# Optimization experiments

Hardware: AMD Instinct MI355X
Metric: run time of the kernel (lower is better)

The kernel has to match this reference:

```python
import jax, jax.numpy as jnp
import numpy as np

N = 50000
E = 1_600_000
D_IN = 128
D_H = 64
D_E = 32
NEG_SLOPE = 0.2


def setup_inputs() -> dict:
    key = jax.random.key(0)
    ks = jax.random.split(key, 20)
    p = lambda k, sh: jax.random.normal(k, sh, jnp.float32) * 0.1
    return {
        "x": jax.random.normal(ks[0], (N, D_IN), jnp.float32),
        "edge_index": jax.random.randint(ks[1], (2, E), 0, N, jnp.int32),
        "edge_attr": jax.random.normal(ks[2], (E, D_E), jnp.float32),
        # layer 1 params (GATv2Conv, heads=1)
        "Wl1": p(ks[3], (D_IN, D_H)), "bl1": p(ks[4], (D_H,)),
        "Wr1": p(ks[5], (D_IN, D_H)), "br1": p(ks[6], (D_H,)),
        "We1": p(ks[7], (D_E, D_H)),
        "att1": p(ks[8], (D_H,)), "bias1": p(ks[9], (D_H,)),
        # layer 2 params
        "Wl2": p(ks[10], (D_H, D_H)), "bl2": p(ks[11], (D_H,)),
        "Wr2": p(ks[12], (D_H, D_H)), "br2": p(ks[13], (D_H,)),
        "We2": p(ks[14], (D_E, D_H)),
        "att2": p(ks[15], (D_H,)), "bias2": p(ks[16], (D_H,)),
        # classifier
        "Wc": p(ks[17], (D_H, 2)), "bc": p(ks[18], (2,)),
    }


def _gatv2(x, src, dst, eattr, Wl, bl, Wr, br, We, att, bias, n):
    # x: [n, d_in]; src/dst: [Ea]; eattr: [Ea, d_e]
    xl = x @ Wl + bl                      # [n, d_h] (source transform; also message value)
    xr = x @ Wr + br                      # [n, d_h] (target transform)
    z = xl[src] + xr[dst] + eattr @ We    # [Ea, d_h]
    score = jax.nn.leaky_relu(z, NEG_SLOPE) @ att  # [Ea]
    # numerically stable softmax over incoming edges per destination node
    m = jax.ops.segment_max(score, dst, num_segments=n)
    ex = jnp.exp(score - m[dst])
    denom = jax.ops.segment_sum(ex, dst, num_segments=n)
    alpha = ex / denom[dst]               # [Ea]
    out = jax.ops.segment_sum(alpha[:, None] * xl[src], dst, num_segments=n)
    return out + bias


def reference(x, edge_index, edge_attr,
              Wl1, bl1, Wr1, br1, We1, att1, bias1,
              Wl2, bl2, Wr2, br2, We2, att2, bias2,
              Wc, bc):
    n = x.shape[0]
    src, dst = edge_index[0], edge_index[1]
    # add self-loops with fill_value='mean' (PyG default with edge_attr):
    # self-loop edge feature of node i = mean of edge_attr over edges into i
    e = edge_attr.shape[0]
    deg = jax.ops.segment_sum(jnp.ones((e,), edge_attr.dtype), dst, num_segments=n)
    loop_attr = jax.ops.segment_sum(edge_attr, dst, num_segments=n) / jnp.maximum(deg, 1.0)[:, None]
    loop = jnp.arange(n, dtype=edge_index.dtype)
    src_a = jnp.concatenate([src, loop])
    dst_a = jnp.concatenate([dst, loop])
    ea = jnp.concatenate([edge_attr, loop_attr], axis=0)

    h = jax.nn.relu(_gatv2(x, src_a, dst_a, ea, Wl1, bl1, Wr1, br1, We1, att1, bias1, n))
    # dropout(p=0.2) is identity in eval mode
    h = jax.nn.relu(_gatv2(h, src_a, dst_a, ea, Wl2, bl2, Wr2, br2, We2, att2, bias2, n))
    return h @ Wc + bc  # [n, 2]
```

## Files before the change

### kernel.cpp

```cpp
#include <hip/hip_runtime.h>
#include <hip/hip_bf16.h>

#define NEG_SLOPE 0.2f

typedef __attribute__((ext_vector_type(8))) short bf16x8;
typedef __attribute__((ext_vector_type(4))) float f32x4;

__device__ __forceinline__ float bf2f(unsigned short u) {
    return __uint_as_float((unsigned)u << 16);
}
__device__ __forceinline__ float bflo(unsigned u) { return __uint_as_float(u << 16); }
__device__ __forceinline__ float bfhi(unsigned u) { return __uint_as_float(u & 0xFFFF0000u); }
__device__ __forceinline__ unsigned short f2bf(float f) {
    unsigned b = __float_as_uint(f);
    return (unsigned short)((b + 0x7FFFu + ((b >> 16) & 1u)) >> 16);
}
__device__ __forceinline__ unsigned pack2(float lo, float hi) {
    return (unsigned)f2bf(lo) | ((unsigned)f2bf(hi) << 16);
}

__global__ void k_hist(const int* __restrict__ dst, int E, int* __restrict__ deg) {
    int e = blockIdx.x * 256 + threadIdx.x;
    if (e < E) atomicAdd(&deg[dst[e]], 1);
}

__global__ __launch_bounds__(1024) void k_scan_chunk(const int* __restrict__ deg,
                                                     int* __restrict__ start,
                                                     int* __restrict__ csum, int n) {
    __shared__ int wsum[16];
    const int lane = threadIdx.x & 63;
    const int w = threadIdx.x >> 6;
    int i = blockIdx.x * 1024 + (int)threadIdx.x;
    int v = (i < n) ? deg[i] : 0;
    int s = v;
#pragma unroll
    for (int o = 1; o < 64; o <<= 1) {
        int u = __shfl_up(s, o);
        if (lane >= o) s += u;
    }
    if (lane == 63) wsum[w] = s;
    __syncthreads();
    if (w == 0) {
        int ws = (lane < 16) ? wsum[lane] : 0;
#pragma unroll
        for (int o = 1; o < 16; o <<= 1) {
            int u = __shfl_up(ws, o);
            if (lane >= o) ws += u;
        }
        if (lane < 16) wsum[lane] = ws;
    }
    __syncthreads();
    int woff = (w == 0) ? 0 : wsum[w - 1];
    int incl = s + woff;
    if (i < n) start[i] = incl - v;
    if (threadIdx.x == 1023) csum[blockIdx.x] = incl;
}

__global__ void k_scan_top(int* __restrict__ csum, int nch, int* __restrict__ start, int n) {
    int t = threadIdx.x;
    int v = (t < nch) ? csum[t] : 0;
    int s = v;
#pragma unroll
    for (int o = 1; o < 64; o <<= 1) {
        int u = __shfl_up(s, o);
        if (t >= o) s += u;
    }
    if (t < nch) csum[t] = s - v;
    if (t == 63) start[n] = s;
}

__global__ void k_scan_apply(int* __restrict__ start, const int* __restrict__ csum, int n) {
    int i = blockIdx.x * 256 + threadIdx.x;
    if (i < n) start[i] += csum[i >> 10];
}

__global__ void k_fill(const float* __restrict__ eattr,
                       const int* __restrict__ src, const int* __restrict__ dst, int E,
                       const int* __restrict__ start, int* __restrict__ cursor,
                       int2* __restrict__ sd_sorted, unsigned short* __restrict__ eattr_s) {
    int e = blockIdx.x * 256 + threadIdx.x;
    if (e >= E) return;
    int d = dst[e];
    int idx = start[d] + atomicAdd(&cursor[d], 1);
    sd_sorted[idx] = make_int2(src[e], d);
    const float4* p = (const float4*)(eattr + (size_t)e * 32);
    uint4* q = (uint4*)(eattr_s + (size_t)idx * 32);
#pragma unroll
    for (int c = 0; c < 4; ++c) {
        const float4 a = p[2 * c], b = p[2 * c + 1];
        uint4 o;
        o.x = pack2(a.x, a.y); o.y = pack2(a.z, a.w);
        o.z = pack2(b.x, b.y); o.w = pack2(b.z, b.w);
        q[c] = o;
    }
}

__global__ __launch_bounds__(256) void k_loop_csr(
    const unsigned short* __restrict__ eattr_s, const int* __restrict__ start,
    float* __restrict__ loop_attr, int n) {
    int node = blockIdx.x * 4 + (threadIdx.x >> 6);
    int t = threadIdx.x & 63;
    if (node >= n) return;
    int a = start[node], b = start[node + 1];
    const int rpi = t >> 4;
    const int cp = t & 15;
    float ax = 0.f, ay = 0.f;
    for (int j = a + rpi; j < b; j += 4) {
        unsigned u = *(const unsigned*)&eattr_s[(size_t)j * 32 + cp * 2];
        ax += bflo(u); ay += bfhi(u);
    }
#pragma unroll
    for (int mask = 16; mask <= 32; mask <<= 1) {
        ax += __shfl_xor(ax, mask);
        ay += __shfl_xor(ay, mask);
    }
    if (t < 16) {
        float deg = fmaxf((float)(b - a), 1.f);
        float2 o = make_float2(ax / deg, ay / deg);
        *(float2*)&loop_attr[(size_t)node * 32 + cp * 2] = o;
    }
}

template <int DIN>
__global__ void k_node_transform(const float* __restrict__ h,
                                 const float* __restrict__ Wl, const float* __restrict__ bl,
                                 const float* __restrict__ Wr, const float* __restrict__ br,
                                 unsigned short* __restrict__ xlb,
                                 unsigned short* __restrict__ xrb, int n) {
    __shared__ float hs[4][DIN];
    int node0 = blockIdx.x * 4;
    int tid = threadIdx.x;
    for (int idx = tid; idx < 4 * DIN; idx += 256) {
        int ln = idx / DIN, k = idx % DIN;
        int node = node0 + ln;
        hs[ln][k] = (node < n) ? h[(long long)node * DIN + k] : 0.f;
    }
    __syncthreads();
    int ln = tid >> 6;
    int j = tid & 63;
    int node = node0 + ln;
    if (node >= n) return;
    float al = bl[j], ar = br[j];
#pragma unroll 8
    for (int k = 0; k < DIN; ++k) {
        float hv = hs[ln][k];
        al += hv * Wl[k * 64 + j];
        ar += hv * Wr[k * 64 + j];
    }
    xlb[(long long)node * 64 + j] = f2bf(al);
    xrb[(long long)node * 64 + j] = f2bf(ar);
}

__global__ __launch_bounds__(256, 2) void k_edge_score(
    const unsigned short* __restrict__ xlb, const unsigned short* __restrict__ xrb,
    const unsigned short* __restrict__ eattr_s,
    const float* __restrict__ We, const float* __restrict__ att,
    const int2* __restrict__ sd_sorted, int E,
    float* __restrict__ ex_sorted) {
    __shared__ __align__(16) short ea_frag[4][128][8];

    const int tid = threadIdx.x;
    const int ge0 = blockIdx.x * 128;
    const int w = tid >> 6, l = tid & 63;
    const int lo16 = l & 15, hi4 = l >> 4;

    int2 sd[2];
#pragma unroll
    for (int et = 0; et < 2; ++et) {
        int ge = ge0 + w * 32 + et * 16 + lo16;
        sd[et] = (ge < E) ? sd_sorted[ge] : make_int2(0, 0);
    }
    uint4 xlg[2][2], xrg[2][2];
#pragma unroll
    for (int et = 0; et < 2; ++et) {
        const size_t lbase = (size_t)sd[et].x * 64 + hi4 * 16;
        const size_t rbase = (size_t)sd[et].y * 64 + hi4 * 16;
        xlg[et][0] = *(const uint4*)&xlb[lbase];
        xlg[et][1] = *(const uint4*)&xlb[lbase + 8];
        xrg[et][0] = *(const uint4*)&xrb[rbase];
        xrg[et][1] = *(const uint4*)&xrb[rbase + 8];
    }

    {
        const int e = tid & 127;
        const int c0 = (tid >> 7) * 2;
        const int ge = ge0 + e;
        uint4 q0 = make_uint4(0, 0, 0, 0), q1 = q0;
        if (ge < E) {
            const uint4* p = (const uint4*)(eattr_s + (size_t)ge * 32 + c0 * 8);
            q0 = p[0]; q1 = p[1];
        }
        *(uint4*)&ea_frag[c0 + 0][e][0] = q0;
        *(uint4*)&ea_frag[c0 + 1][e][0] = q1;
    }

    bf16x8 afrag[4];
#pragma unroll
    for (int ct = 0; ct < 4; ++ct) {
        const int ch = (lo16 >> 2) * 16 + ct * 4 + (lo16 & 3);
#pragma unroll
        for (int j = 0; j < 8; ++j) {
            afrag[ct][j] = (short)f2bf(We[(hi4 * 8 + j) * 64 + ch]);
        }
    }
    float attf[16];
    {
        const float4 a0 = *(const float4*)&att[hi4 * 16 + 0];
        const float4 a1 = *(const float4*)&att[hi4 * 16 + 4];
        const float4 a2 = *(const float4*)&att[hi4 * 16 + 8];
        const float4 a3 = *(const float4*)&att[hi4 * 16 + 12];
        attf[0] = a0.x;  attf[1] = a0.y;  attf[2] = a0.z;  attf[3] = a0.w;
        attf[4] = a1.x;  attf[5] = a1.y;  attf[6] = a1.z;  attf[7] = a1.w;
        attf[8] = a2.x;  attf[9] = a2.y;  attf[10] = a2.z; attf[11] = a2.w;
        attf[12] = a3.x; attf[13] = a3.y; attf[14] = a3.z; attf[15] = a3.w;
    }
    __syncthreads();

    f32x4 acc[2][4];
#pragma unroll
    for (int et = 0; et < 2; ++et) {
        bf16x8 bfrag = *(const bf16x8*)&ea_frag[hi4][w * 32 + et * 16 + lo16][0];
#pragma unroll
        for (int ct = 0; ct < 4; ++ct) {
            f32x4 zero = {0.f, 0.f, 0.f, 0.f};
            acc[et][ct] = __builtin_amdgcn_mfma_f32_16x16x32_bf16(afrag[ct], bfrag, zero, 0, 0, 0);
        }
    }

#pragma unroll
    for (int et = 0; et < 2; ++et) {
        float xlf[16], xrf[16];
#pragma unroll
        for (int h = 0; h < 2; ++h) {
            const uint4 ql = xlg[et][h];
            const uint4 qr = xrg[et][h];
            xlf[h * 8 + 0] = bflo(ql.x); xlf[h * 8 + 1] = bfhi(ql.x);
            xlf[h * 8 + 2] = bflo(ql.y); xlf[h * 8 + 3] = bfhi(ql.y);
            xlf[h * 8 + 4] = bflo(ql.z); xlf[h * 8 + 5] = bfhi(ql.z);
            xlf[h * 8 + 6] = bflo(ql.w); xlf[h * 8 + 7] = bfhi(ql.w);
            xrf[h * 8 + 0] = bflo(qr.x); xrf[h * 8 + 1] = bfhi(qr.x);
            xrf[h * 8 + 2] = bflo(qr.y); xrf[h * 8 + 3] = bfhi(qr.y);
            xrf[h * 8 + 4] = bflo(qr.z); xrf[h * 8 + 5] = bfhi(qr.z);
            xrf[h * 8 + 6] = bflo(qr.w); xrf[h * 8 + 7] = bfhi(qr.w);
        }
        float part = 0.f;
#pragma unroll
        for (int ct = 0; ct < 4; ++ct) {
#pragma unroll
            for (int r = 0; r < 4; ++r) {
                const int i = ct * 4 + r;
                float zz = acc[et][ct][r] + xlf[i] + xrf[i];
                zz = (zz > 0.f) ? zz : NEG_SLOPE * zz;
                part += attf[i] * zz;
            }
        }
        part += __shfl_xor(part, 16);
        part += __shfl_xor(part, 32);
        if (l < 16) {
            int ge = ge0 + w * 32 + et * 16 + l;
            if (ge < E) ex_sorted[ge] = __expf(part);
        }
    }
}

template <bool FINAL>
__global__ __launch_bounds__(256, 2) void k_node_aggr(
    const unsigned short* __restrict__ xlb, const unsigned short* __restrict__ xrb,
    const float* __restrict__ loop_attr,
    const float* __restrict__ We, const float* __restrict__ att,
    const int* __restrict__ start,
    const int2* __restrict__ sd_sorted, const float* __restrict__ ex_sorted,
    const float* __restrict__ bias,
    const float* __restrict__ Wc, const float* __restrict__ bc,
    float* __restrict__ hout, int n) {
    __shared__ float la_s[4][32];
    const int ln = threadIdx.x >> 6;
    const int node = blockIdx.x * 4 + ln;
    const int t = threadIdx.x & 63;

    if (threadIdx.x < 128) {
        int nn = blockIdx.x * 4 + (threadIdx.x >> 5);
        int k = threadIdx.x & 31;
        la_s[threadIdx.x >> 5][k] = (nn < n) ? loop_attr[(size_t)nn * 32 + k] : 0.f;
    }
    __syncthreads();
    if (node >= n) return;

    float exl;
    {
        float zl = bf2f(xlb[(size_t)node * 64 + t]) + bf2f(xrb[(size_t)node * 64 + t]);
#pragma unroll 8
        for (int k = 0; k < 32; ++k) zl += We[k * 64 + t] * la_s[ln][k];
        zl = (zl > 0.f) ? zl : NEG_SLOPE * zl;
        float v = att[t] * zl;
#pragma unroll
        for (int mask = 1; mask <= 32; mask <<= 1) v += __shfl_xor(v, mask);
        exl = __expf(v);
    }

    const int g = t >> 3;
    const int c8 = t & 7;
    int a = start[node], b = start[node + 1];

    float acc[8] = {0.f, 0.f, 0.f, 0.f, 0.f, 0.f, 0.f, 0.f};
    float den = 0.f;
    if (g == 0) {
        const uint4 q = *(const uint4*)&xlb[(size_t)node * 64 + c8 * 8];
        acc[0] = exl * bflo(q.x); acc[1] = exl * bfhi(q.x);
        acc[2] = exl * bflo(q.y); acc[3] = exl * bfhi(q.y);
        acc[4] = exl * bflo(q.z); acc[5] = exl * bfhi(q.z);
        acc[6] = exl * bflo(q.w); acc[7] = exl * bfhi(q.w);
        den = exl;
    }
    for (int j = a; j < b; j += 64) {
        int m = b - j; if (m > 64) m = 64;
        int sj = 0; float exj = 0.f;
        if (t < m) { sj = sd_sorted[j + t].x; exj = ex_sorted[j + t]; }
        for (int i = 0; i < m; i += 16) {
            const int i0 = i + g, i1 = i + 8 + g;
            const int s0 = __shfl(sj, i0); const float e0 = __shfl(exj, i0);
            const int s1 = __shfl(sj, i1); const float e1 = __shfl(exj, i1);
            uint4 q0 = *(const uint4*)&xlb[(size_t)s0 * 64 + c8 * 8];
            uint4 q1 = *(const uint4*)&xlb[(size_t)s1 * 64 + c8 * 8];
            if (i0 < m) {
                acc[0] += e0 * bflo(q0.x); acc[1] += e0 * bfhi(q0.x);
                acc[2] += e0 * bflo(q0.y); acc[3] += e0 * bfhi(q0.y);
                acc[4] += e0 * bflo(q0.z); acc[5] += e0 * bfhi(q0.z);
                acc[6] += e0 * bflo(q0.w); acc[7] += e0 * bfhi(q0.w);
                den += e0;
            }
            if (i1 < m) {
                acc[0] += e1 * bflo(q1.x); acc[1] += e1 * bfhi(q1.x);
                acc[2] += e1 * bflo(q1.y); acc[3] += e1 * bfhi(q1.y);
                acc[4] += e1 * bflo(q1.z); acc[5] += e1 * bfhi(q1.z);
                acc[6] += e1 * bflo(q1.w); acc[7] += e1 * bfhi(q1.w);
                den += e1;
            }
        }
    }
#pragma unroll
    for (int mask = 8; mask <= 32; mask <<= 1) {
#pragma unroll
        for (int r = 0; r < 8; ++r) acc[r] += __shfl_xor(acc[r], mask);
        den += __shfl_xor(den, mask);
    }
    if (!FINAL) {
        if (g == 0) {
            float h[8];
#pragma unroll
            for (int r = 0; r < 8; ++r)
                h[r] = fmaxf(acc[r] / den + bias[c8 * 8 + r], 0.f);
            float4 o0 = make_float4(h[0], h[1], h[2], h[3]);
            float4 o1 = make_float4(h[4], h[5], h[6], h[7]);
            *(float4*)&hout[(size_t)node * 64 + c8 * 8] = o0;
            *(float4*)&hout[(size_t)node * 64 + c8 * 8 + 4] = o1;
        }
    } else {
        float v0 = 0.f, v1 = 0.f;
        if (g == 0) {
#pragma unroll
            for (int r = 0; r < 8; ++r) {
                const int ch = c8 * 8 + r;
                const float h = fmaxf(acc[r] / den + bias[ch], 0.f);
                v0 += h * Wc[ch * 2 + 0];
                v1 += h * Wc[ch * 2 + 1];
            }
        }
#pragma unroll
        for (int mask = 1; mask <= 4; mask <<= 1) {
            v0 += __shfl_xor(v0, mask);
            v1 += __shfl_xor(v1, mask);
        }
        if (t == 0) {
            hout[(size_t)node * 2 + 0] = v0 + bc[0];
            hout[(size_t)node * 2 + 1] = v1 + bc[1];
        }
    }
}

extern "C" void kernel_launch(void* const* d_in, const int* in_sizes, int n_in,
                              void* d_out, int out_size, void* d_ws, size_t ws_size,
                              hipStream_t stream) {
    const float* x     = (const float*)d_in[0];
    const int*   ei    = (const int*)d_in[1];
    const float* eattr = (const float*)d_in[2];
    const float* Wl1 = (const float*)d_in[3];
    const float* bl1 = (const float*)d_in[4];
    const float* Wr1 = (const float*)d_in[5];
    const float* br1 = (const float*)d_in[6];
    const float* We1 = (const float*)d_in[7];
    const float* att1 = (const float*)d_in[8];
    const float* bias1 = (const float*)d_in[9];
    const float* Wl2 = (const float*)d_in[10];
    const float* bl2 = (const float*)d_in[11];
    const float* Wr2 = (const float*)d_in[12];
    const float* br2 = (const float*)d_in[13];
    const float* We2 = (const float*)d_in[14];
    const float* att2 = (const float*)d_in[15];
    const float* bias2 = (const float*)d_in[16];
    const float* Wc = (const float*)d_in[17];
    const float* bc = (const float*)d_in[18];

    const int N = in_sizes[0] / 128;
    const int E = in_sizes[1] / 2;
    const int* src = ei;
    const int* dst = ei + E;

    char* w = (char*)d_ws;
    auto alloc = [&](size_t bytes) {
        char* p = w;
        w += (bytes + 255) & ~(size_t)255;
        return p;
    };
    unsigned short* xlb        = (unsigned short*)alloc((size_t)N * 64 * 2);
    unsigned short* xrb        = (unsigned short*)alloc((size_t)N * 64 * 2);
    float*          hbuf       = (float*)alloc((size_t)N * 64 * 4);
    float*          loop_attr  = (float*)alloc((size_t)N * 32 * 4);
    int*            deg_i      = (int*)alloc((size_t)N * 4);
    int*            start      = (int*)alloc((size_t)(N + 1) * 4);
    int*            cursor     = (int*)alloc((size_t)N * 4);
    int*            csum       = (int*)alloc(256 * 4);
    int2*           sd_sorted  = (int2*)alloc((size_t)E * 8);
    float*          ex_sorted  = (float*)alloc((size_t)E * 4);
    unsigned short* eattr_s    = (unsigned short*)alloc((size_t)E * 32 * 2);

    const int THREADS = 256;
    const int score_blocks = (E + 127) / 128;
    const int node4_blocks = (N + 3) / 4;
    const int edge_blocks = (E + THREADS - 1) / THREADS;
    const int nchunks = (N + 1023) / 1024;

    hipMemsetAsync(deg_i, 0, (size_t)N * 4, stream);
    hipMemsetAsync(cursor, 0, (size_t)N * 4, stream);
    k_hist<<<edge_blocks, THREADS, 0, stream>>>(dst, E, deg_i);
    k_scan_chunk<<<nchunks, 1024, 0, stream>>>(deg_i, start, csum, N);
    k_scan_top<<<1, 64, 0, stream>>>(csum, nchunks, start, N);
    k_scan_apply<<<(N + THREADS - 1) / THREADS, THREADS, 0, stream>>>(start, csum, N);
    k_fill<<<edge_blocks, THREADS, 0, stream>>>(eattr, src, dst, E, start, cursor,
                                                sd_sorted, eattr_s);
    k_loop_csr<<<node4_blocks, THREADS, 0, stream>>>(eattr_s, start, loop_attr, N);

    k_node_transform<128><<<node4_blocks, THREADS, 0, stream>>>(x, Wl1, bl1, Wr1, br1,
                                                                xlb, xrb, N);
    k_edge_score<<<score_blocks, THREADS, 0, stream>>>(
        xlb, xrb, eattr_s, We1, att1, sd_sorted, E, ex_sorted);
    k_node_aggr<false><<<node4_blocks, THREADS, 0, stream>>>(
        xlb, xrb, loop_attr, We1, att1, start, sd_sorted, ex_sorted,
        bias1, Wc, bc, hbuf, N);

    k_node_transform<64><<<node4_blocks, THREADS, 0, stream>>>(hbuf, Wl2, bl2, Wr2, br2,
                                                               xlb, xrb, N);
    k_edge_score<<<score_blocks, THREADS, 0, stream>>>(
        xlb, xrb, eattr_s, We2, att2, sd_sorted, E, ex_sorted);
    k_node_aggr<true><<<node4_blocks, THREADS, 0, stream>>>(
        xlb, xrb, loop_attr, We2, att2, start, sd_sorted, ex_sorted,
        bias2, Wc, bc, (float*)d_out, N);
}
```

Before: 631.8 us.

## Fuse CSR fill and bf16 edge-attr conversion into layer-1 edge scoring

Merges the counting-sort scatter kernel (k_fill) with the first layer's edge score kernel. Each edge's score is computed in original edge order, straight from the fp32 edge attributes and src/dst. The score, src/dst pair and bf16 edge attributes are then scattered to the sorted CSR slot. This removes one full pass that read the edges and then reread the sorted copies, at the cost of uncoalesced scattered writes of ex, sd and eattr. It also gives up the locality that sorted dst order gave the xr gathers. The self-loop mean kernel moves after the fused kernel.

New measurement: 666.7 us. +5.5%, slower.

```diff
diff --git a/kernel.cpp b/kernel.cpp
--- a/kernel.cpp
+++ b/kernel.cpp
@@ -14,9 +14,6 @@
 __device__ __forceinline__ unsigned short f2bf(float f) {
     unsigned b = __float_as_uint(f);
     return (unsigned short)((b + 0x7FFFu + ((b >> 16) & 1u)) >> 16);
-}
-__device__ __forceinline__ unsigned pack2(float lo, float hi) {
-    return (unsigned)f2bf(lo) | ((unsigned)f2bf(hi) << 16);
 }
 
 __global__ void k_hist(const int* __restrict__ dst, int E, int* __restrict__ deg) {
@@ -72,27 +69,6 @@
 __global__ void k_scan_apply(int* __restrict__ start, const int* __restrict__ csum, int n) {
     int i = blockIdx.x * 256 + threadIdx.x;
     if (i < n) start[i] += csum[i >> 10];
-}
-
-__global__ void k_fill(const float* __restrict__ eattr,
-                       const int* __restrict__ src, const int* __restrict__ dst, int E,
-                       const int* __restrict__ start, int* __restrict__ cursor,
-                       int2* __restrict__ sd_sorted, unsigned short* __restrict__ eattr_s) {
-    int e = blockIdx.x * 256 + threadIdx.x;
-    if (e >= E) return;
-    int d = dst[e];
-    int idx = start[d] + atomicAdd(&cursor[d], 1);
-    sd_sorted[idx] = make_int2(src[e], d);
-    const float4* p = (const float4*)(eattr + (size_t)e * 32);
-    uint4* q = (uint4*)(eattr_s + (size_t)idx * 32);
-#pragma unroll
-    for (int c = 0; c < 4; ++c) {
-        const float4 a = p[2 * c], b = p[2 * c + 1];
-        uint4 o;
-        o.x = pack2(a.x, a.y); o.y = pack2(a.z, a.w);
-        o.z = pack2(b.x, b.y); o.w = pack2(b.z, b.w);
-        q[c] = o;
-    }
 }
 
 __global__ __launch_bounds__(256) void k_loop_csr(
@@ -149,6 +125,150 @@
     }
     xlb[(long long)node * 64 + j] = f2bf(al);
     xrb[(long long)node * 64 + j] = f2bf(ar);
+}
+
+__global__ __launch_bounds__(256, 2) void k_edge_score_fill(
+    const unsigned short* __restrict__ xlb, const unsigned short* __restrict__ xrb,
+    const float* __restrict__ eattr,
+    const float* __restrict__ We, const float* __restrict__ att,
+    const int* __restrict__ src, const int* __restrict__ dst,
+    const int* __restrict__ start, int* __restrict__ cursor, int E,
+    float* __restrict__ ex_sorted, int2* __restrict__ sd_sorted,
+    unsigned short* __restrict__ eattr_s) {
+    __shared__ __align__(16) short ea_frag[4][128][8];
+    __shared__ int idx_s[128];
+
+    const int tid = threadIdx.x;
+    const int ge0 = blockIdx.x * 128;
+    const int w = tid >> 6, l = tid & 63;
+    const int lo16 = l & 15, hi4 = l >> 4;
+
+    int sq[2], dq[2];
+#pragma unroll
+    for (int et = 0; et < 2; ++et) {
+        int ge = ge0 + w * 32 + et * 16 + lo16;
+        bool ok = ge < E;
+        sq[et] = ok ? src[ge] : 0;
+        dq[et] = ok ? dst[ge] : 0;
+    }
+    uint4 xlg[2][2], xrg[2][2];
+#pragma unroll
+    for (int et = 0; et < 2; ++et) {
+        const size_t lbase = (size_t)sq[et] * 64 + hi4 * 16;
+        const size_t rbase = (size_t)dq[et] * 64 + hi4 * 16;
+        xlg[et][0] = *(const uint4*)&xlb[lbase];
+        xlg[et][1] = *(const uint4*)&xlb[lbase + 8];
+        xrg[et][0] = *(const uint4*)&xrb[rbase];
+        xrg[et][1] = *(const uint4*)&xrb[rbase + 8];
+    }
+
+    {
+        const int e = tid & 127;
+        const int c0 = (tid >> 7) * 2;
+        const int ge = ge0 + e;
+        float4 a = make_float4(0.f, 0.f, 0.f, 0.f), b = a, c = a, d4 = a;
+        if (ge < E) {
+            const float4* p = (const float4*)(eattr + (size_t)ge * 32 + c0 * 8);
+            a = p[0]; b = p[1]; c = p[2]; d4 = p[3];
+        }
+        bf16x8 lo, hi;
+        lo[0] = (short)f2bf(a.x); lo[1] = (short)f2bf(a.y); lo[2] = (short)f2bf(a.z); lo[3] = (short)f2bf(a.w);
+        lo[4] = (short)f2bf(b.x); lo[5] = (short)f2bf(b.y); lo[6] = (short)f2bf(b.z); lo[7] = (short)f2bf(b.w);
+        hi[0] = (short)f2bf(c.x); hi[1] = (short)f2bf(c.y); hi[2] = (short)f2bf(c.z); hi[3] = (short)f2bf(c.w);
+        hi[4] = (short)f2bf(d4.x); hi[5] = (short)f2bf(d4.y); hi[6] = (short)f2bf(d4.z); hi[7] = (short)f2bf(d4.w);
+        *(bf16x8*)&ea_frag[c0 + 0][e][0] = lo;
+        *(bf16x8*)&ea_frag[c0 + 1][e][0] = hi;
+    }
+
+    bf16x8 afrag[4];
+#pragma unroll
+    for (int ct = 0; ct < 4; ++ct) {
+        const int ch = (lo16 >> 2) * 16 + ct * 4 + (lo16 & 3);
+#pragma unroll
+        for (int j = 0; j < 8; ++j) {
+            afrag[ct][j] = (short)f2bf(We[(hi4 * 8 + j) * 64 + ch]);
+        }
+    }
+    float attf[16];
+    {
+        const float4 a0 = *(const float4*)&att[hi4 * 16 + 0];
+        const float4 a1 = *(const float4*)&att[hi4 * 16 + 4];
+        const float4 a2 = *(const float4*)&att[hi4 * 16 + 8];
+        const float4 a3 = *(const float4*)&att[hi4 * 16 + 12];
+        attf[0] = a0.x;  attf[1] = a0.y;  attf[2] = a0.z;  attf[3] = a0.w;
+        attf[4] = a1.x;  attf[5] = a1.y;  attf[6] = a1.z;  attf[7] = a1.w;
+        attf[8] = a2.x;  attf[9] = a2.y;  attf[10] = a2.z; attf[11] = a2.w;
+        attf[12] = a3.x; attf[13] = a3.y; attf[14] = a3.z; attf[15] = a3.w;
+    }
+    __syncthreads();
+
+    f32x4 acc[2][4];
+#pragma unroll
+    for (int et = 0; et < 2; ++et) {
+        bf16x8 bfrag = *(const bf16x8*)&ea_frag[hi4][w * 32 + et * 16 + lo16][0];
+#pragma unroll
+        for (int ct = 0; ct < 4; ++ct) {
+            f32x4 zero = {0.f, 0.f, 0.f, 0.f};
+            acc[et][ct] = __builtin_amdgcn_mfma_f32_16x16x32_bf16(afrag[ct], bfrag, zero, 0, 0, 0);
+        }
+    }
+
+#pragma unroll
+    for (int et = 0; et < 2; ++et) {
+        float xlf[16], xrf[16];
+#pragma unroll
+        for (int h = 0; h < 2; ++h) {
+            const uint4 ql = xlg[et][h];
+            const uint4 qr = xrg[et][h];
+            xlf[h * 8 + 0] = bflo(ql.x); xlf[h * 8 + 1] = bfhi(ql.x);
+            xlf[h * 8 + 2] = bflo(ql.y); xlf[h * 8 + 3] = bfhi(ql.y);
+            xlf[h * 8 + 4] = bflo(ql.z); xlf[h * 8 + 5] = bfhi(ql.z);
+            xlf[h * 8 + 6] = bflo(ql.w); xlf[h * 8 + 7] = bfhi(ql.w);
+            xrf[h * 8 + 0] = bflo(qr.x); xrf[h * 8 + 1] = bfhi(qr.x);
+            xrf[h * 8 + 2] = bflo(qr.y); xrf[h * 8 + 3] = bfhi(qr.y);
+            xrf[h * 8 + 4] = bflo(qr.z); xrf[h * 8 + 5] = bfhi(qr.z);
+            xrf[h * 8 + 6] = bflo(qr.w); xrf[h * 8 + 7] = bfhi(qr.w);
+        }
+        float part = 0.f;
+#pragma unroll
+        for (int ct = 0; ct < 4; ++ct) {
+#pragma unroll
+            for (int r = 0; r < 4; ++r) {
+                const int i = ct * 4 + r;
+                float zz = acc[et][ct][r] + xlf[i] + xrf[i];
+                zz = (zz > 0.f) ? zz : NEG_SLOPE * zz;
+                part += attf[i] * zz;
+            }
+        }
+        part += __shfl_xor(part, 16);
+        part += __shfl_xor(part, 32);
+        if (l < 16) {
+            const int eb = w * 32 + et * 16 + l;
+            const int ge = ge0 + eb;
+            int idx = -1;
+            if (ge < E) {
+                const int s = sq[et], d = dq[et];
+                idx = start[d] + atomicAdd(&cursor[d], 1);
+                ex_sorted[idx] = __expf(part);
+                sd_sorted[idx] = make_int2(s, d);
+            }
+            idx_s[eb] = idx;
+        }
+    }
+    __syncthreads();
+
+    {
+        const int e = tid >> 1;
+        const int h = tid & 1;
+        const int idx = idx_s[e];
+        if (idx >= 0) {
+            uint4 q0 = *(const uint4*)&ea_frag[h * 2 + 0][e][0];
+            uint4 q1 = *(const uint4*)&ea_frag[h * 2 + 1][e][0];
+            uint4* q = (uint4*)(eattr_s + (size_t)idx * 32 + h * 16);
+            q[0] = q0;
+            q[1] = q1;
+        }
+    }
 }
 
 __global__ __launch_bounds__(256, 2) void k_edge_score(
@@ -436,14 +556,13 @@
     k_scan_chunk<<<nchunks, 1024, 0, stream>>>(deg_i, start, csum, N);
     k_scan_top<<<1, 64, 0, stream>>>(csum, nchunks, start, N);
     k_scan_apply<<<(N + THREADS - 1) / THREADS, THREADS, 0, stream>>>(start, csum, N);
-    k_fill<<<edge_blocks, THREADS, 0, stream>>>(eattr, src, dst, E, start, cursor,
-                                                sd_sorted, eattr_s);
-    k_loop_csr<<<node4_blocks, THREADS, 0, stream>>>(eattr_s, start, loop_attr, N);
 
     k_node_transform<128><<<node4_blocks, THREADS, 0, stream>>>(x, Wl1, bl1, Wr1, br1,
                                                                 xlb, xrb, N);
-    k_edge_score<<<score_blocks, THREADS, 0, stream>>>(
-        xlb, xrb, eattr_s, We1, att1, sd_sorted, E, ex_sorted);
+    k_edge_score_fill<<<score_blocks, THREADS, 0, stream>>>(
+        xlb, xrb, eattr, We1, att1, src, dst, start, cursor, E,
+        ex_sorted, sd_sorted, eattr_s);
+    k_loop_csr<<<node4_blocks, THREADS, 0, stream>>>(eattr_s, start, loop_attr, N);
     k_node_aggr<false><<<node4_blocks, THREADS, 0, stream>>>(
         xlb, xrb, loop_attr, We1, att1, start, sd_sorted, ex_sorted,
         bias1, Wc, bc, hbuf, N);
```
